# Kernel tuning notes

Measured on AMD Instinct MI355X. Metric: run time of the kernel, lower is better.

## Reference

```python
import jax, jax.numpy as jnp
import numpy as np

R, S, D, V, K, B, L, U, I = 20000, 64, 128, 50000, 32, 2048, 20480, 100000, 100000


def setup_inputs() -> dict:
    key = jax.random.key(0)
    ks = jax.random.split(key, 16)
    # segment ids: equal-sized history per batch element (guaranteed non-empty)
    seg = (jnp.arange(L, dtype=jnp.int32) // (L // B)).astype(jnp.int32)
    return {
        "user": jax.random.randint(ks[0], (B,), 0, U, dtype=jnp.int32),
        "item": jax.random.randint(ks[1], (B,), 0, I, dtype=jnp.int32),
        "historical_review": jax.random.randint(ks[2], (R, S), 0, V, dtype=jnp.int32),
        "historical_review_positive": jax.random.normal(ks[3], (R, D), jnp.float32),
        "user_hist_idx": jax.random.randint(ks[4], (L,), 0, R, dtype=jnp.int32),
        "user_hist_seg": seg,
        "item_hist_idx": jax.random.randint(ks[5], (L,), 0, R, dtype=jnp.int32),
        "item_hist_seg": seg,
        "word_emb": jax.random.normal(ks[6], (V, D), jnp.float32) * 0.02,
        "M_w": jax.random.normal(ks[7], (D, D), jnp.float32) * (1.0 / np.sqrt(D)),
        "M_b": jnp.zeros((D,), jnp.float32),
        "W_w": jax.random.normal(ks[8], (D, K), jnp.float32) * (1.0 / np.sqrt(D)),
        "W_b": jnp.zeros((K,), jnp.float32),
        "T_w": jax.random.normal(ks[9], (K, D), jnp.float32) * (1.0 / np.sqrt(K)),
        "T_b": jnp.zeros((D,), jnp.float32),
        "user_emb": jax.random.normal(ks[10], (U, D), jnp.float32) * 0.02,
        "item_emb": jax.random.normal(ks[11], (I, D), jnp.float32) * 0.02,
        "avg_rating": jnp.full((1,), 3.5, jnp.float32),
    }


def _segment_mean(x, seg, num_segments):
    s = jax.ops.segment_sum(x, seg, num_segments=num_segments)
    c = jax.ops.segment_sum(jnp.ones(seg.shape, x.dtype), seg, num_segments=num_segments)
    return s / jnp.maximum(c, 1.0)[:, None]


def reference(user, item, historical_review, historical_review_positive,
              user_hist_idx, user_hist_seg, item_hist_idx, item_hist_seg,
              word_emb, M_w, M_b, W_w, W_b, T_w, T_b,
              user_emb, item_emb, avg_rating):
    # --- aspect extraction (ABAE-style) over R historical reviews ---
    e_w = word_emb[historical_review]                      # [R, S, D] gather
    y_s = historical_review_positive                       # [R, D] sentence embedding
    # dx = transform_M(e_w) @ y_s  -> attention logits over words
    dx = jnp.einsum('rsd,de,re->rs', e_w, M_w, y_s) + jnp.einsum('d,rd->r', M_b, y_s)[:, None]
    ax = jax.nn.softmax(dx, axis=1)                        # [R, S]
    z_s = jnp.einsum('rsd,rs->rd', e_w, ax)                # [R, D]
    p_t = jax.nn.softmax(z_s @ W_w + W_b, axis=1)          # [R, K] aspect probs
    r_s = p_t @ T_w + T_b                                  # [R, D] aspect-based review embedding
    # --- ragged gather + mean-pool over user/item histories ---
    ua = _segment_mean(r_s[user_hist_idx], user_hist_seg, B)  # [B, D]
    ia = _segment_mean(r_s[item_hist_idx], item_hist_seg, B)  # [B, D]
    uf = user_emb[user]                                    # [B, D]
    itf = item_emb[item]                                   # [B, D]
    prediction = jnp.sum(ua * ia, axis=-1) + jnp.sum(uf * itf, axis=-1) + avg_rating[0]
    return prediction  # [B]
```

## Files before the change

### kernel.cpp

```cpp
#include <hip/hip_runtime.h>


typedef __attribute__((ext_vector_type(8))) short bf16x8;
typedef __attribute__((ext_vector_type(4))) float f32x4;
typedef __attribute__((ext_vector_type(2))) float vf2;

__device__ __forceinline__ unsigned int f2bf_rne(float x) {
  unsigned int u = __float_as_uint(x);
  return (u + 0x7fffu + ((u >> 16) & 1u)) >> 16;
}
__device__ __forceinline__ float bf_lo(unsigned int w) { return __uint_as_float(w << 16); }
__device__ __forceinline__ float bf_hi(unsigned int w) { return __uint_as_float(w & 0xffff0000u); }

__global__ __launch_bounds__(256) void kA_mfma(
    const float* __restrict__ We, const float* __restrict__ Mw,
    const float* __restrict__ Ww, unsigned char* __restrict__ Z, int V) {
  __shared__ uint4 Bs[2560];
  int t = threadIdx.x;
  int L = t & 63, wid = t >> 6;

#pragma unroll
  for (int q = 0; q < 10; ++q) {
    int c = t + q * 256;
    int cl = c & 63, g = c >> 6;
    int jt = g >> 2, ks = g & 3;
    int n = jt * 16 + (cl & 15);
    int k0 = ks * 32 + (cl >> 4) * 8;
    float v[8];
#pragma unroll
    for (int j = 0; j < 8; ++j) {
      int e = k0 + j;
      v[j] = (n < 128) ? Mw[(size_t)e * 128 + n] : Ww[(size_t)e * 32 + (n - 128)];
    }
    uint4 pk;
    pk.x = f2bf_rne(v[0]) | (f2bf_rne(v[1]) << 16);
    pk.y = f2bf_rne(v[2]) | (f2bf_rne(v[3]) << 16);
    pk.z = f2bf_rne(v[4]) | (f2bf_rne(v[5]) << 16);
    pk.w = f2bf_rne(v[6]) | (f2bf_rne(v[7]) << 16);
    Bs[c] = pk;
  }
  __syncthreads();

  int r0 = blockIdx.x * 64;
  if (r0 > V - 64) r0 = V - 64;
  int rowA = r0 + wid * 16 + (L & 15);
  const float4* Arow = (const float4*)(We + (size_t)rowA * 128);

  f32x4 acc[10];
#pragma unroll
  for (int jt = 0; jt < 10; ++jt) acc[jt] = (f32x4){0.f, 0.f, 0.f, 0.f};

#pragma unroll
  for (int ks = 0; ks < 4; ++ks) {
    int koff4 = ks * 8 + (L >> 4) * 2;
    float4 a0 = Arow[koff4];
    float4 a1 = Arow[koff4 + 1];
    union { uint4 u; bf16x8 v; } A;
    A.u.x = f2bf_rne(a0.x) | (f2bf_rne(a0.y) << 16);
    A.u.y = f2bf_rne(a0.z) | (f2bf_rne(a0.w) << 16);
    A.u.z = f2bf_rne(a1.x) | (f2bf_rne(a1.y) << 16);
    A.u.w = f2bf_rne(a1.z) | (f2bf_rne(a1.w) << 16);
#pragma unroll
    for (int jt = 0; jt < 10; ++jt) {
      union { uint4 u; bf16x8 v; } Bf;
      Bf.u = Bs[(jt * 4 + ks) * 64 + L];
      acc[jt] = __builtin_amdgcn_mfma_f32_16x16x32_bf16(A.v, Bf.v, acc[jt], 0, 0, 0);
    }
  }

#pragma unroll
  for (int jt = 0; jt < 8; ++jt) {
#pragma unroll
    for (int i = 0; i < 4; ++i) {
      float v0 = acc[jt][i] * 64.f;
      float v1 = __shfl_xor(v0, 1);
      float v2 = __shfl_xor(v0, 2);
      float v3 = __shfl_xor(v0, 3);
      if (!(L & 3)) {
        int col = jt * 16 + (L & 15);
        int orow = r0 + wid * 16 + (L >> 4) * 4 + i;
        int w8 = __builtin_amdgcn_cvt_pk_fp8_f32(v0, v1, 0, false);
        w8 = __builtin_amdgcn_cvt_pk_fp8_f32(v2, v3, w8, true);
        *(int*)(Z + (size_t)orow * 192 + col) = w8;
      }
    }
  }
#pragma unroll
  for (int jt = 8; jt < 10; ++jt) {
#pragma unroll
    for (int i = 0; i < 4; ++i) {
      unsigned int u = f2bf_rne(acc[jt][i]);
      unsigned int partner = (unsigned int)__shfl_xor((int)u, 1);
      if (!(L & 1)) {
        int k = (jt - 8) * 16 + (L & 15);
        int orow = r0 + wid * 16 + (L >> 4) * 4 + i;
        *(unsigned int*)(Z + (size_t)orow * 192 + 128 + k * 2) = u | (partner << 16);
      }
    }
  }
}

__device__ __forceinline__ float dot_fp8_16(uint4 q, const float4* y) {
  float s = 0.f;
#pragma unroll
  for (int i = 0; i < 4; ++i) {
    unsigned int u = (&q.x)[i];
    vf2 a = __builtin_amdgcn_cvt_pk_f32_fp8(u, false);
    vf2 b = __builtin_amdgcn_cvt_pk_f32_fp8(u, true);
    float4 yv = y[i];
    s += a.x * yv.x + a.y * yv.y + b.x * yv.z + b.y * yv.w;
  }
  return s;
}

__global__ __launch_bounds__(256) void k3_review(
    const int* __restrict__ hr, const float* __restrict__ Y,
    const unsigned char* __restrict__ Z, const float* __restrict__ Wb,
    const float* __restrict__ Tw, const float* __restrict__ Tb,
    float* __restrict__ rs, int R) {
  int t = threadIdx.x;
  int wv = t >> 6, lane = t & 63;
  int r = blockIdx.x * 4 + wv;
  if (r >= R) r = R - 1;

  int word = hr[(size_t)r * 64 + lane];
  int g = lane & 15, sub = lane >> 4;

  const unsigned char* bp[4];
#pragma unroll
  for (int p = 0; p < 4; ++p) {
    int wid = __shfl(word, p * 16 + g);
    bp[p] = Z + (size_t)wid * 192;
  }
  uint4 q0[4], q1[4], w8[4];
#pragma unroll
  for (int p = 0; p < 4; ++p) {
    q0[p] = *(const uint4*)(bp[p] + sub * 16);
    q1[p] = *(const uint4*)(bp[p] + 64 + sub * 16);
    w8[p] = *(const uint4*)(bp[p] + 128 + sub * 16);
  }
  const float4* Yr = (const float4*)(Y + (size_t)r * 128);
  float4 ya[4], yb[4];
#pragma unroll
  for (int i = 0; i < 4; ++i) {
    ya[i] = Yr[sub * 4 + i];
    yb[i] = Yr[16 + sub * 4 + i];
  }

  float dxp[4];
#pragma unroll
  for (int p = 0; p < 4; ++p) {
    float acc = dot_fp8_16(q0[p], ya) + dot_fp8_16(q1[p], yb);
    acc += __shfl_xor(acc, 16);
    acc += __shfl_xor(acc, 32);
    dxp[p] = acc * 0.015625f;
  }
  float dx = dxp[0];
  dx = (sub == 1) ? dxp[1] : dx;
  dx = (sub == 2) ? dxp[2] : dx;
  dx = (sub == 3) ? dxp[3] : dx;

  float m = dx;
#pragma unroll
  for (int off = 32; off; off >>= 1) m = fmaxf(m, __shfl_xor(m, off));
  float ex = __expf(dx - m);
  float sum = ex;
#pragma unroll
  for (int off = 32; off; off >>= 1) sum += __shfl_xor(sum, off);
  float ax = ex / sum;

  float lacc[8];
#pragma unroll
  for (int j = 0; j < 8; ++j) lacc[j] = 0.f;
#pragma unroll
  for (int p = 0; p < 4; ++p) {
    float axp = __shfl(ax, p * 16 + g);
#pragma unroll
    for (int j = 0; j < 8; ++j) {
      unsigned int u = (&w8[p].x)[j >> 1];
      float wwv = (j & 1) ? bf_hi(u) : bf_lo(u);
      lacc[j] += axp * wwv;
    }
  }
#pragma unroll
  for (int off = 8; off; off >>= 1) {
#pragma unroll
    for (int j = 0; j < 8; ++j) lacc[j] += __shfl_xor(lacc[j], off);
  }
  const float4* Wb4 = (const float4*)Wb;
  float4 wba = Wb4[sub * 2], wbb = Wb4[sub * 2 + 1];
  lacc[0] += wba.x; lacc[1] += wba.y; lacc[2] += wba.z; lacc[3] += wba.w;
  lacc[4] += wbb.x; lacc[5] += wbb.y; lacc[6] += wbb.z; lacc[7] += wbb.w;

  float mk = lacc[0];
#pragma unroll
  for (int j = 1; j < 8; ++j) mk = fmaxf(mk, lacc[j]);
  mk = fmaxf(mk, __shfl_xor(mk, 16));
  mk = fmaxf(mk, __shfl_xor(mk, 32));
  float ek[8], sk = 0.f;
#pragma unroll
  for (int j = 0; j < 8; ++j) { ek[j] = __expf(lacc[j] - mk); sk += ek[j]; }
  sk += __shfl_xor(sk, 16);
  sk += __shfl_xor(sk, 32);
  float inv = 1.0f / sk;
  float pv[8];
#pragma unroll
  for (int j = 0; j < 8; ++j) pv[j] = ek[j] * inv;

  const float2* T2 = (const float2*)Tw;
  float2 acc2 = ((const float2*)Tb)[lane];
#pragma unroll
  for (int kk = 0; kk < 32; ++kk) {
    float pk = __shfl(pv[kk & 7], (kk >> 3) * 16);
    float2 tv = T2[kk * 64 + lane];
    acc2.x += pk * tv.x;
    acc2.y += pk * tv.y;
  }
  ((float2*)rs)[(size_t)r * 64 + lane] = acc2;
}

__global__ __launch_bounds__(256) void k4_final(
    const float* __restrict__ rs, const int* __restrict__ uidx,
    const int* __restrict__ iidx, const int* __restrict__ user,
    const int* __restrict__ item, const float* __restrict__ uemb,
    const float* __restrict__ iemb, const float* __restrict__ avg,
    float* __restrict__ out, int B, int per) {
  int t = threadIdx.x;
  int w = t >> 6, lane = t & 63;
  int b = blockIdx.x * 4 + w;
  if (b >= B) return;
  const float2* rs2 = (const float2*)rs;
  float2 ua = {0.f, 0.f}, ia = {0.f, 0.f};
  int base = b * per;
  for (int j = 0; j < per; ++j) {
    int id = uidx[base + j];
    float2 tv = rs2[(size_t)id * 64 + lane];
    ua.x += tv.x; ua.y += tv.y;
  }
  for (int j = 0; j < per; ++j) {
    int id = iidx[base + j];
    float2 tv = rs2[(size_t)id * 64 + lane];
    ia.x += tv.x; ia.y += tv.y;
  }
  float inv = 1.0f / (float)per;
  float part = (ua.x * ia.x + ua.y * ia.y) * inv * inv;
  float2 uf = ((const float2*)uemb)[(size_t)user[b] * 64 + lane];
  float2 itf = ((const float2*)iemb)[(size_t)item[b] * 64 + lane];
  part += uf.x * itf.x + uf.y * itf.y;
#pragma unroll
  for (int off = 32; off; off >>= 1) part += __shfl_xor(part, off);
  if (lane == 0) out[b] = part + avg[0];
}

extern "C" void kernel_launch(void* const* d_in, const int* in_sizes, int n_in,
                              void* d_out, int out_size, void* d_ws, size_t ws_size,
                              hipStream_t stream) {
  const int*   user = (const int*)d_in[0];
  const int*   item = (const int*)d_in[1];
  const int*   hr   = (const int*)d_in[2];
  const float* Y    = (const float*)d_in[3];
  const int*   uhi  = (const int*)d_in[4];
  const int*   ihi  = (const int*)d_in[6];
  const float* We   = (const float*)d_in[8];
  const float* Mw   = (const float*)d_in[9];
  const float* Ww   = (const float*)d_in[11];
  const float* Wb   = (const float*)d_in[12];
  const float* Tw   = (const float*)d_in[13];
  const float* Tb   = (const float*)d_in[14];
  const float* Ue   = (const float*)d_in[15];
  const float* Ie   = (const float*)d_in[16];
  const float* avg  = (const float*)d_in[17];

  int B = in_sizes[0];
  int R = in_sizes[3] / 128;
  int V = in_sizes[8] / 128;
  int L = in_sizes[4];
  int per = L / B;

  unsigned char* Z = (unsigned char*)d_ws;
  float* rsbuf = (float*)(Z + (size_t)V * 192);
  float* out = (float*)d_out;

  kA_mfma<<<(V + 63) / 64, 256, 0, stream>>>(We, Mw, Ww, Z, V);
  k3_review<<<(R + 3) / 4, 256, 0, stream>>>(hr, Y, Z, Wb, Tw, Tb, rsbuf, R);
  k4_final<<<(B + 3) / 4, 256, 0, stream>>>(rsbuf, uhi, ihi, user, item, Ue, Ie, avg, out, B, per);
}
```

Before: 238.0 us.

## Pack weights once in a prelude kernel and store word-aspect logits as fp8

A new small kernel converts M_w and W_w to packed bf16 once, so each of the ~780 MFMA blocks copies pre-packed tiles into LDS instead of gathering and converting fp32 weights itself. The per-word aspect logits (e_w·W_w) are now stored as scaled fp8 in a separate 32-byte-per-word table instead of bf16 inside a 192-byte row, and the M-projection table shrinks to 128 bytes per word. This cuts gather traffic and row size in the review kernel, at the cost of lower precision on the aspect logits and one extra kernel launch.

```diff
diff --git a/kernel.cpp b/kernel.cpp
--- a/kernel.cpp
+++ b/kernel.cpp
@@ -9,36 +9,39 @@
   unsigned int u = __float_as_uint(x);
   return (u + 0x7fffu + ((u >> 16) & 1u)) >> 16;
 }
-__device__ __forceinline__ float bf_lo(unsigned int w) { return __uint_as_float(w << 16); }
-__device__ __forceinline__ float bf_hi(unsigned int w) { return __uint_as_float(w & 0xffff0000u); }
+
+__global__ __launch_bounds__(256) void kA0_pack(
+    const float* __restrict__ Mw, const float* __restrict__ Ww,
+    uint4* __restrict__ Wpk) {
+  int c = blockIdx.x * 256 + threadIdx.x;
+  if (c >= 2560) return;
+  int cl = c & 63, g = c >> 6;
+  int jt = g >> 2, ks = g & 3;
+  int n = jt * 16 + (cl & 15);
+  int k0 = ks * 32 + (cl >> 4) * 8;
+  float v[8];
+#pragma unroll
+  for (int j = 0; j < 8; ++j) {
+    int e = k0 + j;
+    v[j] = (n < 128) ? Mw[(size_t)e * 128 + n] : Ww[(size_t)e * 32 + (n - 128)];
+  }
+  uint4 pk;
+  pk.x = f2bf_rne(v[0]) | (f2bf_rne(v[1]) << 16);
+  pk.y = f2bf_rne(v[2]) | (f2bf_rne(v[3]) << 16);
+  pk.z = f2bf_rne(v[4]) | (f2bf_rne(v[5]) << 16);
+  pk.w = f2bf_rne(v[6]) | (f2bf_rne(v[7]) << 16);
+  Wpk[c] = pk;
+}
 
 __global__ __launch_bounds__(256) void kA_mfma(
-    const float* __restrict__ We, const float* __restrict__ Mw,
-    const float* __restrict__ Ww, unsigned char* __restrict__ Z, int V) {
+    const float* __restrict__ We, const uint4* __restrict__ Wpk,
+    unsigned char* __restrict__ Z, unsigned char* __restrict__ WW8, int V) {
   __shared__ uint4 Bs[2560];
   int t = threadIdx.x;
   int L = t & 63, wid = t >> 6;
 
 #pragma unroll
-  for (int q = 0; q < 10; ++q) {
-    int c = t + q * 256;
-    int cl = c & 63, g = c >> 6;
-    int jt = g >> 2, ks = g & 3;
-    int n = jt * 16 + (cl & 15);
-    int k0 = ks * 32 + (cl >> 4) * 8;
-    float v[8];
-#pragma unroll
-    for (int j = 0; j < 8; ++j) {
-      int e = k0 + j;
-      v[j] = (n < 128) ? Mw[(size_t)e * 128 + n] : Ww[(size_t)e * 32 + (n - 128)];
-    }
-    uint4 pk;
-    pk.x = f2bf_rne(v[0]) | (f2bf_rne(v[1]) << 16);
-    pk.y = f2bf_rne(v[2]) | (f2bf_rne(v[3]) << 16);
-    pk.z = f2bf_rne(v[4]) | (f2bf_rne(v[5]) << 16);
-    pk.w = f2bf_rne(v[6]) | (f2bf_rne(v[7]) << 16);
-    Bs[c] = pk;
-  }
+  for (int q = 0; q < 10; ++q) Bs[t + q * 256] = Wpk[t + q * 256];
   __syncthreads();
 
   int r0 = blockIdx.x * 64;
@@ -69,7 +72,7 @@
   }
 
 #pragma unroll
-  for (int jt = 0; jt < 8; ++jt) {
+  for (int jt = 0; jt < 10; ++jt) {
 #pragma unroll
     for (int i = 0; i < 4; ++i) {
       float v0 = acc[jt][i] * 64.f;
@@ -81,20 +84,10 @@
         int orow = r0 + wid * 16 + (L >> 4) * 4 + i;
         int w8 = __builtin_amdgcn_cvt_pk_fp8_f32(v0, v1, 0, false);
         w8 = __builtin_amdgcn_cvt_pk_fp8_f32(v2, v3, w8, true);
-        *(int*)(Z + (size_t)orow * 192 + col) = w8;
-      }
-    }
-  }
-#pragma unroll
-  for (int jt = 8; jt < 10; ++jt) {
-#pragma unroll
-    for (int i = 0; i < 4; ++i) {
-      unsigned int u = f2bf_rne(acc[jt][i]);
-      unsigned int partner = (unsigned int)__shfl_xor((int)u, 1);
-      if (!(L & 1)) {
-        int k = (jt - 8) * 16 + (L & 15);
-        int orow = r0 + wid * 16 + (L >> 4) * 4 + i;
-        *(unsigned int*)(Z + (size_t)orow * 192 + 128 + k * 2) = u | (partner << 16);
+        if (col < 128)
+          *(int*)(Z + (size_t)orow * 128 + col) = w8;
+        else
+          *(int*)(WW8 + (size_t)orow * 32 + (col - 128)) = w8;
       }
     }
   }
@@ -115,9 +108,9 @@
 
 __global__ __launch_bounds__(256) void k3_review(
     const int* __restrict__ hr, const float* __restrict__ Y,
-    const unsigned char* __restrict__ Z, const float* __restrict__ Wb,
-    const float* __restrict__ Tw, const float* __restrict__ Tb,
-    float* __restrict__ rs, int R) {
+    const unsigned char* __restrict__ Z, const unsigned char* __restrict__ WW8,
+    const float* __restrict__ Wb, const float* __restrict__ Tw,
+    const float* __restrict__ Tb, float* __restrict__ rs, int R) {
   int t = threadIdx.x;
   int wv = t >> 6, lane = t & 63;
   int r = blockIdx.x * 4 + wv;
@@ -126,18 +119,18 @@
   int word = hr[(size_t)r * 64 + lane];
   int g = lane & 15, sub = lane >> 4;
 
-  const unsigned char* bp[4];
+  int wid_p[4];
+#pragma unroll
+  for (int p = 0; p < 4; ++p) wid_p[p] = __shfl(word, p * 16 + g);
+
+  uint4 q0[4], q1[4];
+  uint2 w8[4];
 #pragma unroll
   for (int p = 0; p < 4; ++p) {
-    int wid = __shfl(word, p * 16 + g);
-    bp[p] = Z + (size_t)wid * 192;
-  }
-  uint4 q0[4], q1[4], w8[4];
-#pragma unroll
-  for (int p = 0; p < 4; ++p) {
-    q0[p] = *(const uint4*)(bp[p] + sub * 16);
-    q1[p] = *(const uint4*)(bp[p] + 64 + sub * 16);
-    w8[p] = *(const uint4*)(bp[p] + 128 + sub * 16);
+    const unsigned char* bp = Z + (size_t)wid_p[p] * 128;
+    q0[p] = *(const uint4*)(bp + sub * 16);
+    q1[p] = *(const uint4*)(bp + 64 + sub * 16);
+    w8[p] = *(const uint2*)(WW8 + (size_t)wid_p[p] * 32 + sub * 8);
   }
   const float4* Yr = (const float4*)(Y + (size_t)r * 128);
   float4 ya[4], yb[4];
@@ -175,12 +168,14 @@
 #pragma unroll
   for (int p = 0; p < 4; ++p) {
     float axp = __shfl(ax, p * 16 + g);
-#pragma unroll
-    for (int j = 0; j < 8; ++j) {
-      unsigned int u = (&w8[p].x)[j >> 1];
-      float wwv = (j & 1) ? bf_hi(u) : bf_lo(u);
-      lacc[j] += axp * wwv;
-    }
+    vf2 a0 = __builtin_amdgcn_cvt_pk_f32_fp8(w8[p].x, false);
+    vf2 a1 = __builtin_amdgcn_cvt_pk_f32_fp8(w8[p].x, true);
+    vf2 a2 = __builtin_amdgcn_cvt_pk_f32_fp8(w8[p].y, false);
+    vf2 a3 = __builtin_amdgcn_cvt_pk_f32_fp8(w8[p].y, true);
+    lacc[0] += axp * a0.x; lacc[1] += axp * a0.y;
+    lacc[2] += axp * a1.x; lacc[3] += axp * a1.y;
+    lacc[4] += axp * a2.x; lacc[5] += axp * a2.y;
+    lacc[6] += axp * a3.x; lacc[7] += axp * a3.y;
   }
 #pragma unroll
   for (int off = 8; off; off >>= 1) {
@@ -189,8 +184,10 @@
   }
   const float4* Wb4 = (const float4*)Wb;
   float4 wba = Wb4[sub * 2], wbb = Wb4[sub * 2 + 1];
-  lacc[0] += wba.x; lacc[1] += wba.y; lacc[2] += wba.z; lacc[3] += wba.w;
-  lacc[4] += wbb.x; lacc[5] += wbb.y; lacc[6] += wbb.z; lacc[7] += wbb.w;
+  lacc[0] = lacc[0] * 0.015625f + wba.x; lacc[1] = lacc[1] * 0.015625f + wba.y;
+  lacc[2] = lacc[2] * 0.015625f + wba.z; lacc[3] = lacc[3] * 0.015625f + wba.w;
+  lacc[4] = lacc[4] * 0.015625f + wbb.x; lacc[5] = lacc[5] * 0.015625f + wbb.y;
+  lacc[6] = lacc[6] * 0.015625f + wbb.z; lacc[7] = lacc[7] * 0.015625f + wbb.w;
 
   float mk = lacc[0];
 #pragma unroll
@@ -277,11 +274,15 @@
   int L = in_sizes[4];
   int per = L / B;
 
-  unsigned char* Z = (unsigned char*)d_ws;
-  float* rsbuf = (float*)(Z + (size_t)V * 192);
+  unsigned char* ws = (unsigned char*)d_ws;
+  uint4* Wpk = (uint4*)ws;
+  unsigned char* Z   = ws + 40960;
+  unsigned char* WW8 = Z + (size_t)V * 128;
+  float* rsbuf = (float*)(WW8 + (size_t)V * 32);
   float* out = (float*)d_out;
 
-  kA_mfma<<<(V + 63) / 64, 256, 0, stream>>>(We, Mw, Ww, Z, V);
-  k3_review<<<(R + 3) / 4, 256, 0, stream>>>(hr, Y, Z, Wb, Tw, Tb, rsbuf, R);
+  kA0_pack<<<10, 256, 0, stream>>>(Mw, Ww, Wpk);
+  kA_mfma<<<(V + 63) / 64, 256, 0, stream>>>(We, Wpk, Z, WW8, V);
+  k3_review<<<(R + 3) / 4, 256, 0, stream>>>(hr, Y, Z, WW8, Wb, Tw, Tb, rsbuf, R);
   k4_final<<<(B + 3) / 4, 256, 0, stream>>>(rsbuf, uhi, ihi, user, item, Ue, Ie, avg, out, B, per);
 }
```

Measured after the change: 237.8 us. Within noise of the previous version (-0.1%).
